# Performance work log

Hardware: AMD Instinct MI355X
Metric: run time of the kernel (lower is better)

## Reference

```python
import jax, jax.numpy as jnp
import numpy as np
import math

D_MODEL = 2048
K = 64
W = 512              # window_size
STRIDE = W // 2      # = 256
EMA_ALPHA = 0.9
N_RETRIEVE = 8
EPS = 1e-12


def _build_cheby(k, w):
    # cheby_mat[k, n] = cos(k * arccos(t_n)), t_n = cos(pi*(2n+1)/(2w))
    ns = np.arange(w, dtype=np.float64)
    t = np.cos(np.pi * (2 * ns + 1) / (2 * w))
    ks = np.arange(k, dtype=np.float64)
    return jnp.asarray(np.cos(ks[:, None] * np.arccos(t)[None, :]), dtype=jnp.float32)


def setup_inputs() -> dict:
    key = jax.random.key(0)
    ks = jax.random.split(key, 5)
    B, S = 2, 8192
    scan_out = jax.random.normal(ks[0], (B, S, D_MODEL), dtype=jnp.float32)
    buf = jax.random.normal(ks[1], (W, D_MODEL), dtype=jnp.float32)  # pre-filled circular buffer
    # unit-modulus random-phase complex roles: r_k[d] = exp(i*theta)
    phases = jax.random.uniform(ks[2], (K, D_MODEL), dtype=jnp.float32) * (2.0 * math.pi)
    roles_real = jnp.cos(phases)
    roles_imag = jnp.sin(phases)
    w_bands = 1.0 / (jnp.arange(K, dtype=jnp.float32) + 1.0)  # w_init = 1/(k+1)
    retrieve_proj_w = jax.random.normal(ks[3], (D_MODEL, D_MODEL), dtype=jnp.float32) * 0.02
    inject_gate = jnp.zeros((1,), dtype=jnp.float32)
    cheby_mat = _build_cheby(K, W)
    return dict(scan_out=scan_out, buf=buf, roles_real=roles_real, roles_imag=roles_imag,
                w_bands=w_bands, retrieve_proj_w=retrieve_proj_w, inject_gate=inject_gate,
                cheby_mat=cheby_mat)


def reference(scan_out, buf, roles_real, roles_imag, w_bands, retrieve_proj_w, inject_gate, cheby_mat):
    S = scan_out.shape[1]
    h_mean = scan_out.mean(axis=0)                      # [S, D] batch-mean like torch code
    n_chunks = S // STRIDE
    chunks = h_mean.reshape(n_chunks, STRIDE, D_MODEL)  # each chunk triggers one bind

    init = (buf, jnp.int32(0),
            jnp.zeros((K, D_MODEL), jnp.float32),   # c_past
            jnp.zeros((D_MODEL,), jnp.float32),     # V_mem_real
            jnp.zeros((D_MODEL,), jnp.float32),     # V_mem_imag
            jnp.zeros((K,), jnp.float32),           # _coeff_norms (EMA)
            jnp.zeros((K,), jnp.float32))           # spectral_delta

    def step(carry, chunk):
        b, pos, c_past, vr, vi, cnorms, _ = carry
        # circular-buffer write of `stride` tokens starting at pos
        b = jax.lax.dynamic_update_slice(b, chunk, (pos, 0))
        pos = (pos + STRIDE) % W
        order = (jnp.arange(W, dtype=jnp.int32) + pos) % W   # oldest-first reorder
        data = b[order]                                      # [W, D]
        # Chebyshev coefficients: c = (2/W) * cheby_mat @ data, c0 halved
        coeffs = (2.0 / W) * (cheby_mat @ data)              # [K, D]
        coeffs = coeffs.at[0].multiply(0.5)
        # HRR-normalized bind into holographic memory via EMA
        norms = jnp.maximum(jnp.linalg.norm(coeffs, axis=-1, keepdims=True), EPS)
        cn = coeffs / norms
        cnorms = EMA_ALPHA * cnorms + (1.0 - EMA_ALPHA) * norms[:, 0]
        vr = EMA_ALPHA * vr + (1.0 - EMA_ALPHA) * (cn * roles_real).sum(axis=0)
        vi = EMA_ALPHA * vi + (1.0 - EMA_ALPHA) * (cn * roles_imag).sum(axis=0)
        # spectral delta vs previous window's coefficients
        delta = jnp.linalg.norm(coeffs - c_past, axis=-1)    # [K]
        return (b, pos, coeffs, vr, vi, cnorms, delta), None

    (b, pos, c_now, vr, vi, cnorms, delta), _ = jax.lax.scan(step, init, chunks)

    # retrieve: unbind top-J bands by spectral delta, denormalize, weight, project
    _, top = jax.lax.top_k(delta, N_RETRIEVE)                # [J]
    rr = roles_real[top]
    ri = roles_imag[top]
    retrieved = (vr[None, :] * rr + vi[None, :] * ri) * jnp.maximum(cnorms[top], EPS)[:, None]  # [J, D]
    weights = jax.nn.softplus(w_bands[top])                  # [J]
    ctx = (weights[:, None] * retrieved).sum(axis=0)         # [D]
    out = (ctx @ retrieve_proj_w.T) * jax.nn.sigmoid(inject_gate[0])  # [D]
    return out, delta, vr, vi
```

## Files before the change

### kernel.cpp

```cpp
#include <hip/hip_runtime.h>
#include <math.h>

#define D_MODEL 2048
#define KB_ 64
#define NCHUNK 32

typedef __bf16 bf16;
typedef __attribute__((ext_vector_type(8))) __bf16 bf16x8;
typedef __attribute__((ext_vector_type(4))) __bf16 bf16x4;
typedef __attribute__((ext_vector_type(4))) float f32x4;

#define OFF_PQ 0
#define N_PQ (33 * 128 * 2048)
#define OFF_CHEB2 N_PQ
#define OFF_NORMS (N_PQ + 16384)
#define OFF_PARTR (OFF_NORMS + 2048)
#define OFF_PARTI (OFF_PARTR + 32 * 2048)
#define OFF_VR (OFF_PARTI + 32 * 2048)
#define OFF_VI (OFF_VR + 2048)
#define OFF_CTX (OFF_VI + 2048)

__global__ __launch_bounds__(256) void k0_prep(
    const float* __restrict__ cheby, bf16* __restrict__ cheb2)
{
  int flat = blockIdx.x * 256 + threadIdx.x;
  int b = flat >> 8, n = flat & 255;
  float v = (b < 64) ? cheby[b * 512 + n] : cheby[(b - 64) * 512 + 256 + n];
  cheb2[flat] = (bf16)v;
}

__global__ __launch_bounds__(256, 2) void k1_mfma(
    const float* __restrict__ scan, const float* __restrict__ buf,
    const bf16* __restrict__ cheb2, float* __restrict__ PQ)
{
  __shared__ bf16 As[128 * 72];
  __shared__ bf16 Bs[128 * 72];

  const int t = threadIdx.x;
  const int dtile = blockIdx.x, j = blockIdx.y;
  const int wid = t >> 6, lane = t & 63;
  const int wm = wid >> 1, wn = wid & 1;
  const int quad = lane >> 4, r16 = lane & 15;
  const int d0 = dtile * 128;
  const float* scan1 = scan + 8192 * 2048;

  f32x4 acc[4][4];
#pragma unroll
  for (int a = 0; a < 4; ++a)
#pragma unroll
    for (int b = 0; b < 4; ++b) acc[a][b] = (f32x4){0.f, 0.f, 0.f, 0.f};

  for (int nb = 0; nb < 4; ++nb) {
    __syncthreads();
#pragma unroll
    for (int i = 0; i < 4; ++i) {
      int flat = t + i * 256;
      int b = flat >> 3, q8 = flat & 7;
      bf16x8 v = *(const bf16x8*)(cheb2 + b * 256 + nb * 64 + q8 * 8);
      *(bf16x8*)(As + b * 72 + q8 * 8) = v;
    }
#pragma unroll
    for (int i = 0; i < 8; ++i) {
      int p = t + i * 256;
      int d = p & 127;
      int n0 = (p >> 7) * 4;
      float v[4];
      if (j == 0) {
#pragma unroll
        for (int x = 0; x < 4; ++x)
          v[x] = buf[(256 + nb * 64 + n0 + x) * 2048 + d0 + d];
      } else {
        int base = ((j - 1) * 256 + nb * 64 + n0) * 2048 + d0 + d;
#pragma unroll
        for (int x = 0; x < 4; ++x)
          v[x] = 0.5f * (scan[base + x * 2048] + scan1[base + x * 2048]);
      }
      bf16x4 e = {(bf16)v[0], (bf16)v[1], (bf16)v[2], (bf16)v[3]};
      *(bf16x4*)(Bs + d * 72 + n0) = e;
    }
    __syncthreads();

#pragma unroll
    for (int ks = 0; ks < 2; ++ks) {
      bf16x8 af[4], bfr[4];
#pragma unroll
      for (int tm = 0; tm < 4; ++tm)
        af[tm] = *(const bf16x8*)(As + (wm * 64 + tm * 16 + r16) * 72 + ks * 32 + quad * 8);
#pragma unroll
      for (int tn = 0; tn < 4; ++tn)
        bfr[tn] = *(const bf16x8*)(Bs + (wn * 64 + tn * 16 + r16) * 72 + ks * 32 + quad * 8);
#pragma unroll
      for (int tm = 0; tm < 4; ++tm)
#pragma unroll
        for (int tn = 0; tn < 4; ++tn)
          acc[tm][tn] = __builtin_amdgcn_mfma_f32_16x16x32_bf16(
              af[tm], bfr[tn], acc[tm][tn], 0, 0, 0);
    }
  }

  const float scale = 2.0f / 512.0f;
#pragma unroll
  for (int tm = 0; tm < 4; ++tm) {
    int band_base = wm * 64 + tm * 16 + quad * 4;
#pragma unroll
    for (int tn = 0; tn < 4; ++tn) {
      int dc = d0 + wn * 64 + tn * 16 + r16;
#pragma unroll
      for (int r = 0; r < 4; ++r) {
        int band = band_base + r;
        float sc = (band == 0 || band == 64) ? scale * 0.5f : scale;
        PQ[(j * 128 + band) * 2048 + dc] = acc[tm][tn][r] * sc;
      }
    }
  }
}

__global__ __launch_bounds__(256) void k2_norms(
    const float* __restrict__ PQ, float* __restrict__ norms,
    float* __restrict__ dout)
{
  const int tid = threadIdx.x;
  const int b = blockIdx.x;
  float s = 0.f;
  if (b < NCHUNK * KB_) {
    int c = b >> 6, k = b & 63;
    const float* P = PQ + (c * 128 + k) * 2048;
    const float* Q = PQ + ((c + 1) * 128 + 64 + k) * 2048;
#pragma unroll
    for (int i = 0; i < 2; ++i) {
      float4 p = *(const float4*)(P + tid * 4 + i * 1024);
      float4 q = *(const float4*)(Q + tid * 4 + i * 1024);
      float x = p.x + q.x, y = p.y + q.y, z = p.z + q.z, w = p.w + q.w;
      s += x * x + y * y + z * z + w * w;
    }
  } else {
    int k = b - NCHUNK * KB_;
    const float* P1 = PQ + (31 * 128 + k) * 2048;
    const float* Q2 = PQ + (32 * 128 + 64 + k) * 2048;
    const float* P0 = PQ + (30 * 128 + k) * 2048;
    const float* Q1 = PQ + (31 * 128 + 64 + k) * 2048;
#pragma unroll
    for (int i = 0; i < 2; ++i) {
      float4 a = *(const float4*)(P1 + tid * 4 + i * 1024);
      float4 bb = *(const float4*)(Q2 + tid * 4 + i * 1024);
      float4 cc = *(const float4*)(P0 + tid * 4 + i * 1024);
      float4 dd = *(const float4*)(Q1 + tid * 4 + i * 1024);
      float x = a.x + bb.x - cc.x - dd.x, y = a.y + bb.y - cc.y - dd.y;
      float z = a.z + bb.z - cc.z - dd.z, w = a.w + bb.w - cc.w - dd.w;
      s += x * x + y * y + z * z + w * w;
    }
  }
  for (int o = 32; o > 0; o >>= 1) s += __shfl_down(s, o, 64);
  __shared__ float red[4];
  if ((tid & 63) == 0) red[tid >> 6] = s;
  __syncthreads();
  if (tid == 0) {
    float r = sqrtf(red[0] + red[1] + red[2] + red[3]);
    if (b < NCHUNK * KB_) norms[b] = fmaxf(r, 1e-12f);
    else dout[D_MODEL + (b - NCHUNK * KB_)] = r;
  }
}

__global__ __launch_bounds__(256) void k3_bind(
    const float* __restrict__ PQ, const float* __restrict__ norms,
    const float* __restrict__ rr, const float* __restrict__ ri,
    float* __restrict__ part_r, float* __restrict__ part_i)
{
  const int d = blockIdx.x * 256 + threadIdx.x;
  const int c = blockIdx.y;
  float wc = 0.1f * powf(0.9f, (float)(31 - c));
  float ar = 0.f, ai = 0.f;
  for (int k = 0; k < KB_; ++k) {
    float coeff = PQ[(c * 128 + k) * 2048 + d] + PQ[((c + 1) * 128 + 64 + k) * 2048 + d];
    float cn = coeff / norms[c * KB_ + k];
    ar += cn * rr[k * D_MODEL + d];
    ai += cn * ri[k * D_MODEL + d];
  }
  part_r[c * D_MODEL + d] = wc * ar;
  part_i[c * D_MODEL + d] = wc * ai;
}

__global__ __launch_bounds__(256) void k3b_reduce(
    const float* __restrict__ part_r, const float* __restrict__ part_i,
    float* __restrict__ vr, float* __restrict__ vi)
{
  const int d = blockIdx.x * 256 + threadIdx.x;
  float sr = 0.f, si = 0.f;
  for (int c = 0; c < NCHUNK; ++c) {
    sr += part_r[c * D_MODEL + d];
    si += part_i[c * D_MODEL + d];
  }
  vr[d] = sr;
  vi[d] = si;
}

__global__ __launch_bounds__(256) void k5a_ctx(
    const float* __restrict__ norms, const float* __restrict__ vr_ws,
    const float* __restrict__ vi_ws, const float* __restrict__ rr,
    const float* __restrict__ ri, const float* __restrict__ wbands,
    float* __restrict__ dout, float* __restrict__ ctx)
{
  __shared__ float cn_s[64];
  __shared__ float del_s[64];
  __shared__ int top_s[8];
  __shared__ float wgt_s[8];
  const int tid = threadIdx.x;
  if (tid < 64) {
    float s = 0.f;
    for (int c = 0; c < NCHUNK; ++c) s = 0.9f * s + 0.1f * norms[c * KB_ + tid];
    cn_s[tid] = s;
    del_s[tid] = dout[D_MODEL + tid];
  }
  __syncthreads();
  if (tid == 0) {
    unsigned long long taken = 0ULL;
    for (int jj = 0; jj < 8; ++jj) {
      float best = -1.f;
      int bi = 0;
      for (int k = 0; k < 64; ++k) {
        if (!((taken >> k) & 1ULL) && del_s[k] > best) { best = del_s[k]; bi = k; }
      }
      taken |= (1ULL << bi);
      top_s[jj] = bi;
      wgt_s[jj] = log1pf(expf(wbands[bi]));
    }
  }
  __syncthreads();
  for (int d = tid; d < D_MODEL; d += 256) {
    float vr = vr_ws[d], vi = vi_ws[d];
    dout[D_MODEL + KB_ + d] = vr;
    dout[D_MODEL + KB_ + D_MODEL + d] = vi;
    float cx = 0.f;
#pragma unroll
    for (int jj = 0; jj < 8; ++jj) {
      int k = top_s[jj];
      cx += wgt_s[jj] * (vr * rr[k * D_MODEL + d] + vi * ri[k * D_MODEL + d]) *
            fmaxf(cn_s[k], 1e-12f);
    }
    ctx[d] = cx;
  }
}

__global__ __launch_bounds__(256) void k5b_gemv(
    const float* __restrict__ Wp, const float* __restrict__ ctx,
    const float* __restrict__ gate, float* __restrict__ dout)
{
  const int tid = threadIdx.x;
  const int lane = tid & 63;
  const int w = tid >> 6;
  const int row = blockIdx.x * 4 + w;
  const float* p = Wp + row * D_MODEL;
  float s = 0.f;
#pragma unroll
  for (int i = 0; i < 8; ++i) {
    int e = lane * 4 + i * 256;
    float4 wv = *(const float4*)(p + e);
    float4 cv = *(const float4*)(ctx + e);
    s += wv.x * cv.x + wv.y * cv.y + wv.z * cv.z + wv.w * cv.w;
  }
  for (int o = 32; o > 0; o >>= 1) s += __shfl_down(s, o, 64);
  if (lane == 0) {
    float sig = 1.f / (1.f + expf(-gate[0]));
    dout[row] = s * sig;
  }
}

extern "C" void kernel_launch(void* const* d_in, const int* in_sizes, int n_in,
                              void* d_out, int out_size, void* d_ws, size_t ws_size,
                              hipStream_t stream) {
  const float* scan  = (const float*)d_in[0];
  const float* buf   = (const float*)d_in[1];
  const float* rr    = (const float*)d_in[2];
  const float* ri    = (const float*)d_in[3];
  const float* wb    = (const float*)d_in[4];
  const float* Wp    = (const float*)d_in[5];
  const float* gate  = (const float*)d_in[6];
  const float* cheby = (const float*)d_in[7];
  float* out = (float*)d_out;
  float* ws = (float*)d_ws;

  float* PQ     = ws + OFF_PQ;
  bf16*  cheb2  = (bf16*)(ws + OFF_CHEB2);
  float* norms  = ws + OFF_NORMS;
  float* part_r = ws + OFF_PARTR;
  float* part_i = ws + OFF_PARTI;
  float* vr     = ws + OFF_VR;
  float* vi     = ws + OFF_VI;
  float* ctx    = ws + OFF_CTX;

  k0_prep<<<128, 256, 0, stream>>>(cheby, cheb2);
  k1_mfma<<<dim3(16, 33), 256, 0, stream>>>(scan, buf, cheb2, PQ);
  k2_norms<<<NCHUNK * KB_ + KB_, 256, 0, stream>>>(PQ, norms, out);
  k3_bind<<<dim3(8, NCHUNK), 256, 0, stream>>>(PQ, norms, rr, ri, part_r, part_i);
  k3b_reduce<<<8, 256, 0, stream>>>(part_r, part_i, vr, vi);
  k5a_ctx<<<1, 256, 0, stream>>>(norms, vr, vi, rr, ri, wb, out, ctx);
  k5b_gemv<<<512, 256, 0, stream>>>(Wp, ctx, gate, out);
}
```

Before: 309.2 us.

## Fuse chebyshev prep into MFMA load, merge reduce into ctx, vectorize bind

After: 301.8 us. 2.4% less time.

```diff
diff --git a/kernel.cpp b/kernel.cpp
--- a/kernel.cpp
+++ b/kernel.cpp
@@ -12,26 +12,14 @@
 
 #define OFF_PQ 0
 #define N_PQ (33 * 128 * 2048)
-#define OFF_CHEB2 N_PQ
-#define OFF_NORMS (N_PQ + 16384)
+#define OFF_NORMS N_PQ
 #define OFF_PARTR (OFF_NORMS + 2048)
 #define OFF_PARTI (OFF_PARTR + 32 * 2048)
-#define OFF_VR (OFF_PARTI + 32 * 2048)
-#define OFF_VI (OFF_VR + 2048)
-#define OFF_CTX (OFF_VI + 2048)
-
-__global__ __launch_bounds__(256) void k0_prep(
-    const float* __restrict__ cheby, bf16* __restrict__ cheb2)
-{
-  int flat = blockIdx.x * 256 + threadIdx.x;
-  int b = flat >> 8, n = flat & 255;
-  float v = (b < 64) ? cheby[b * 512 + n] : cheby[(b - 64) * 512 + 256 + n];
-  cheb2[flat] = (bf16)v;
-}
-
-__global__ __launch_bounds__(256, 2) void k1_mfma(
+#define OFF_CTX (OFF_PARTI + 32 * 2048)
+
+__global__ __launch_bounds__(256, 4) void k1_mfma(
     const float* __restrict__ scan, const float* __restrict__ buf,
-    const bf16* __restrict__ cheb2, float* __restrict__ PQ)
+    const float* __restrict__ cheby, float* __restrict__ PQ)
 {
   __shared__ bf16 As[128 * 72];
   __shared__ bf16 Bs[128 * 72];
@@ -53,11 +41,14 @@
   for (int nb = 0; nb < 4; ++nb) {
     __syncthreads();
 #pragma unroll
-    for (int i = 0; i < 4; ++i) {
+    for (int i = 0; i < 8; ++i) {
       int flat = t + i * 256;
-      int b = flat >> 3, q8 = flat & 7;
-      bf16x8 v = *(const bf16x8*)(cheb2 + b * 256 + nb * 64 + q8 * 8);
-      *(bf16x8*)(As + b * 72 + q8 * 8) = v;
+      int b = flat >> 4, q4 = flat & 15;
+      const float* src = (b < 64) ? (cheby + b * 512 + nb * 64)
+                                  : (cheby + (b - 64) * 512 + 256 + nb * 64);
+      float4 v = *(const float4*)(src + q4 * 4);
+      bf16x4 e = {(bf16)v.x, (bf16)v.y, (bf16)v.z, (bf16)v.w};
+      *(bf16x4*)(As + b * 72 + q4 * 4) = e;
     }
 #pragma unroll
     for (int i = 0; i < 8; ++i) {
@@ -166,50 +157,43 @@
     const float* __restrict__ rr, const float* __restrict__ ri,
     float* __restrict__ part_r, float* __restrict__ part_i)
 {
-  const int d = blockIdx.x * 256 + threadIdx.x;
+  const int d4 = (blockIdx.x * 256 + threadIdx.x) * 4;
   const int c = blockIdx.y;
-  float wc = 0.1f * powf(0.9f, (float)(31 - c));
-  float ar = 0.f, ai = 0.f;
+  const float wc = 0.1f * powf(0.9f, (float)(31 - c));
+  float4 ar = make_float4(0.f, 0.f, 0.f, 0.f);
+  float4 ai = make_float4(0.f, 0.f, 0.f, 0.f);
   for (int k = 0; k < KB_; ++k) {
-    float coeff = PQ[(c * 128 + k) * 2048 + d] + PQ[((c + 1) * 128 + 64 + k) * 2048 + d];
-    float cn = coeff / norms[c * KB_ + k];
-    ar += cn * rr[k * D_MODEL + d];
-    ai += cn * ri[k * D_MODEL + d];
-  }
-  part_r[c * D_MODEL + d] = wc * ar;
-  part_i[c * D_MODEL + d] = wc * ai;
-}
-
-__global__ __launch_bounds__(256) void k3b_reduce(
-    const float* __restrict__ part_r, const float* __restrict__ part_i,
-    float* __restrict__ vr, float* __restrict__ vi)
-{
-  const int d = blockIdx.x * 256 + threadIdx.x;
-  float sr = 0.f, si = 0.f;
-  for (int c = 0; c < NCHUNK; ++c) {
-    sr += part_r[c * D_MODEL + d];
-    si += part_i[c * D_MODEL + d];
-  }
-  vr[d] = sr;
-  vi[d] = si;
-}
-
-__global__ __launch_bounds__(256) void k5a_ctx(
-    const float* __restrict__ norms, const float* __restrict__ vr_ws,
-    const float* __restrict__ vi_ws, const float* __restrict__ rr,
+    float4 p = *(const float4*)(PQ + (c * 128 + k) * 2048 + d4);
+    float4 q = *(const float4*)(PQ + ((c + 1) * 128 + 64 + k) * 2048 + d4);
+    float inv = 1.0f / norms[c * KB_ + k];
+    float4 r = *(const float4*)(rr + k * D_MODEL + d4);
+    float4 im = *(const float4*)(ri + k * D_MODEL + d4);
+    float cx = (p.x + q.x) * inv, cy = (p.y + q.y) * inv;
+    float cz = (p.z + q.z) * inv, cw = (p.w + q.w) * inv;
+    ar.x += cx * r.x; ar.y += cy * r.y; ar.z += cz * r.z; ar.w += cw * r.w;
+    ai.x += cx * im.x; ai.y += cy * im.y; ai.z += cz * im.z; ai.w += cw * im.w;
+  }
+  float4 outr = make_float4(wc * ar.x, wc * ar.y, wc * ar.z, wc * ar.w);
+  float4 outi = make_float4(wc * ai.x, wc * ai.y, wc * ai.z, wc * ai.w);
+  *(float4*)(part_r + c * D_MODEL + d4) = outr;
+  *(float4*)(part_i + c * D_MODEL + d4) = outi;
+}
+
+__global__ __launch_bounds__(256) void k4_ctx(
+    const float* __restrict__ norms, const float* __restrict__ part_r,
+    const float* __restrict__ part_i, const float* __restrict__ rr,
     const float* __restrict__ ri, const float* __restrict__ wbands,
     float* __restrict__ dout, float* __restrict__ ctx)
 {
   __shared__ float cn_s[64];
-  __shared__ float del_s[64];
   __shared__ int top_s[8];
   __shared__ float wgt_s[8];
   const int tid = threadIdx.x;
+  const int d = blockIdx.x * 256 + tid;
   if (tid < 64) {
     float s = 0.f;
     for (int c = 0; c < NCHUNK; ++c) s = 0.9f * s + 0.1f * norms[c * KB_ + tid];
-    cn_s[tid] = s;
-    del_s[tid] = dout[D_MODEL + tid];
+    cn_s[tid] = fmaxf(s, 1e-12f);
   }
   __syncthreads();
   if (tid == 0) {
@@ -218,7 +202,8 @@
       float best = -1.f;
       int bi = 0;
       for (int k = 0; k < 64; ++k) {
-        if (!((taken >> k) & 1ULL) && del_s[k] > best) { best = del_s[k]; bi = k; }
+        float dv = dout[D_MODEL + k];
+        if (!((taken >> k) & 1ULL) && dv > best) { best = dv; bi = k; }
       }
       taken |= (1ULL << bi);
       top_s[jj] = bi;
@@ -226,19 +211,20 @@
     }
   }
   __syncthreads();
-  for (int d = tid; d < D_MODEL; d += 256) {
-    float vr = vr_ws[d], vi = vi_ws[d];
-    dout[D_MODEL + KB_ + d] = vr;
-    dout[D_MODEL + KB_ + D_MODEL + d] = vi;
-    float cx = 0.f;
-#pragma unroll
-    for (int jj = 0; jj < 8; ++jj) {
-      int k = top_s[jj];
-      cx += wgt_s[jj] * (vr * rr[k * D_MODEL + d] + vi * ri[k * D_MODEL + d]) *
-            fmaxf(cn_s[k], 1e-12f);
-    }
-    ctx[d] = cx;
-  }
+  float sr = 0.f, si = 0.f;
+  for (int c = 0; c < NCHUNK; ++c) {
+    sr += part_r[c * D_MODEL + d];
+    si += part_i[c * D_MODEL + d];
+  }
+  dout[D_MODEL + KB_ + d] = sr;
+  dout[D_MODEL + KB_ + D_MODEL + d] = si;
+  float cx = 0.f;
+#pragma unroll
+  for (int jj = 0; jj < 8; ++jj) {
+    int k = top_s[jj];
+    cx += wgt_s[jj] * (sr * rr[k * D_MODEL + d] + si * ri[k * D_MODEL + d]) * cn_s[k];
+  }
+  ctx[d] = cx;
 }
 
 __global__ __launch_bounds__(256) void k5b_gemv(
@@ -280,19 +266,14 @@
   float* ws = (float*)d_ws;
 
   float* PQ     = ws + OFF_PQ;
-  bf16*  cheb2  = (bf16*)(ws + OFF_CHEB2);
   float* norms  = ws + OFF_NORMS;
   float* part_r = ws + OFF_PARTR;
   float* part_i = ws + OFF_PARTI;
-  float* vr     = ws + OFF_VR;
-  float* vi     = ws + OFF_VI;
   float* ctx    = ws + OFF_CTX;
 
-  k0_prep<<<128, 256, 0, stream>>>(cheby, cheb2);
-  k1_mfma<<<dim3(16, 33), 256, 0, stream>>>(scan, buf, cheb2, PQ);
+  k1_mfma<<<dim3(16, 33), 256, 0, stream>>>(scan, buf, cheby, PQ);
   k2_norms<<<NCHUNK * KB_ + KB_, 256, 0, stream>>>(PQ, norms, out);
-  k3_bind<<<dim3(8, NCHUNK), 256, 0, stream>>>(PQ, norms, rr, ri, part_r, part_i);
-  k3b_reduce<<<8, 256, 0, stream>>>(part_r, part_i, vr, vi);
-  k5a_ctx<<<1, 256, 0, stream>>>(norms, vr, vi, rr, ri, wb, out, ctx);
+  k3_bind<<<dim3(2, NCHUNK), 256, 0, stream>>>(PQ, norms, rr, ri, part_r, part_i);
+  k4_ctx<<<8, 256, 0, stream>>>(norms, part_r, part_i, rr, ri, wb, out, ctx);
   k5b_gemv<<<512, 256, 0, stream>>>(Wp, ctx, gate, out);
 }
```
